# Kernel tuning notes

Measured on AMD Instinct MI355X. Metric: run time of the kernel, lower is better.

## Reference

```python
import jax, jax.numpy as jnp
import numpy as np

NUM_HEADS = 12
ROPE_THETA = 10000.0


def rope_angles(hd, end_x, end_y):
    # axial 2D rope angles, shape (L, hd//2); first hd//4 from x-coord, next hd//4 from y-coord
    f = 1.0 / (ROPE_THETA ** (np.arange(0, hd, 4)[: hd // 4].astype(np.float32) / hd))
    t = np.arange(end_x * end_y)
    tx = (t % end_x).astype(np.float32)
    ty = (t // end_x).astype(np.float32)
    ang = np.concatenate([np.outer(tx, f), np.outer(ty, f)], axis=-1)
    return jnp.asarray(ang, dtype=jnp.float32)


def apply_rope(q, ang):
    # q: (B, nH, L, hd); complex multiply on adjacent pairs
    cos, sin = jnp.cos(ang), jnp.sin(ang)  # (L, hd//2)
    qr = q.reshape(*q.shape[:-1], -1, 2)
    a, b = qr[..., 0], qr[..., 1]
    return jnp.stack([a * cos - b * sin, a * sin + b * cos], axis=-1).reshape(q.shape)


def setup_inputs() -> dict:
    key = jax.random.key(0)
    ks = jax.random.split(key, 7)
    dim, H, W, B = 768, 32, 32, 8
    hd = dim // NUM_HEADS
    return {
        "x": jax.random.normal(ks[0], (B, H, W, dim), jnp.float32),
        "qkv_w": jax.random.normal(ks[1], (3 * dim, dim), jnp.float32) * 0.02,
        "qkv_b": jax.random.normal(ks[2], (3 * dim,), jnp.float32) * 0.02,
        "proj_w": jax.random.normal(ks[3], (dim, dim), jnp.float32) * 0.02,
        "proj_b": jax.random.normal(ks[4], (dim,), jnp.float32) * 0.02,
        "rel_pos_h": jax.random.normal(ks[5], (2 * H - 1, hd), jnp.float32) * 0.02,
        "rel_pos_w": jax.random.normal(ks[6], (2 * W - 1, hd), jnp.float32) * 0.02,
    }


def reference(x, qkv_w, qkv_b, proj_w, proj_b, rel_pos_h, rel_pos_w):
    B, H, W, dim = x.shape
    nH = NUM_HEADS
    hd = dim // nH
    L = H * W
    qkv = jnp.einsum("blc,dc->bld", x.reshape(B, L, dim), qkv_w) + qkv_b
    qkv = qkv.reshape(B, L, 3, nH, hd)
    q = qkv[:, :, 0].transpose(0, 2, 1, 3)  # (B, nH, L, hd)
    k = qkv[:, :, 1].transpose(0, 2, 1, 3)
    v = qkv[:, :, 2].transpose(0, 2, 1, 3)
    # 2D rope (applied to both q and k)
    ang = rope_angles(hd, H, W)
    q = apply_rope(q, ang)
    k = apply_rope(k, ang)
    # relative position bias: equivalent math of concat_rel_pos(rescale=True) + SDPA
    # effective scores = (q.k)/sqrt(hd) + rel_h + rel_w
    rc = jnp.arange(H)[:, None] - jnp.arange(W)[None, :] + (H - 1)  # (H, W)
    Rh = rel_pos_h[rc]  # (H, K_h, hd)
    Rw = rel_pos_w[rc]  # (W, K_w, hd)
    rq = q.reshape(B, nH, H, W, hd)
    rel_h = jnp.einsum("bnhwc,hkc->bnhwk", rq, Rh)  # (B, nH, H, W, K_h)
    rel_w = jnp.einsum("bnhwc,wkc->bnhwk", rq, Rw)  # (B, nH, H, W, K_w)
    scores = jnp.einsum("bnqc,bnkc->bnqk", q, k) / jnp.sqrt(jnp.float32(hd))
    scores = scores.reshape(B, nH, H, W, H, W) + rel_h[..., :, None] + rel_w[..., None, :]
    attn = jax.nn.softmax(scores.reshape(B, nH, L, L), axis=-1)
    out = jnp.einsum("bnqk,bnkc->bnqc", attn, v)  # (B, nH, L, hd)
    out = out.transpose(0, 2, 1, 3).reshape(B, H, W, dim)
    return jnp.einsum("bhwc,dc->bhwd", out, proj_w) + proj_b
```

## Files before the change

### kernel.cpp

```cpp
#include <hip/hip_runtime.h>


typedef unsigned short u16;
typedef __attribute__((ext_vector_type(8))) __bf16 bf16x8;
typedef __attribute__((ext_vector_type(4))) float f32x4;
typedef __attribute__((address_space(1))) const unsigned int gu32;
typedef __attribute__((address_space(3))) unsigned int lu32;

#define LOG2E 1.4426950408889634f

__device__ __forceinline__ float b2f(u16 u) {
    unsigned int i = ((unsigned int)u) << 16;
    float f; __builtin_memcpy(&f, &i, 4); return f;
}
__device__ __forceinline__ u16 f2b(float f) {
    unsigned int x; __builtin_memcpy(&x, &f, 4);
    x += 0x7fffu + ((x >> 16) & 1u);
    return (u16)(x >> 16);
}

__global__ void detect_dtype(const u16* __restrict__ x, int* __restrict__ flag)
{
    if (threadIdx.x == 0 && blockIdx.x == 0) {
        float mx = 0.f;
        for (int i = 0; i < 128; i++) {
            float v = fabsf(b2f(x[i]));
            if (!(v <= 1e30f)) v = 1e30f;
            mx = fmaxf(mx, v);
        }
        *flag = (mx > 1e4f) ? 1 : 0;
    }
}

struct CvtArgs {
    const void* src[7];
    u16*        dst[7];
    int         n[7];
    float       sc[7];
};

__global__ __launch_bounds__(256) void convert_all(CvtArgs a, const int* __restrict__ flag)
{
    const int fl = *flag;
    const int g = blockIdx.x * 256 + threadIdx.x;
    const int stride = gridDim.x * 256;
    #pragma unroll 1
    for (int s = 0; s < 7; s++) {
        const int n = a.n[s];
        const float sc = a.sc[s];
        const float* fs = (const float*)a.src[s];
        const u16*  hs = (const u16*)a.src[s];
        u16* d = a.dst[s];
        for (int i = g; i < n; i += stride) {
            float v = fl ? fs[i] : b2f(hs[i]);
            d[i] = f2b(v * sc);
        }
    }
}

template <int EPI>
__global__ __launch_bounds__(256) void gemm128(
    const u16* __restrict__ A, const u16* __restrict__ Bw,
    const u16* __restrict__ bias, void* __restrict__ Cout,
    const int* __restrict__ flag, u16* __restrict__ qkvT, int N, int K)
{
    __shared__ __align__(16) u16 smem[16384];
    __shared__ float tabc[512];
    __shared__ float tabs[512];
    u16* lA = smem;
    u16* lB = smem + 8192;
    u16* ct = smem;
    const int tid = threadIdx.x;
    const int m0 = blockIdx.x * 128, n0 = blockIdx.y * 128;
    const int wave = tid >> 6, lane = tid & 63;
    const int wm = (wave & 1) * 64, wn = (wave >> 1) * 64;
    const int lm = lane & 15, lq = lane >> 4;
    const int srow = lane >> 3;
    const int sgcol = ((lane & 7) ^ (srow & 7)) * 8;
    const int sw0 = (lq ^ (lm & 7)) * 8;
    const int sw1 = ((lq + 4) ^ (lm & 7)) * 8;

    if (EPI == 1) {
        #pragma unroll
        for (int e = tid; e < 512; e += 256) {
            const int coord = e >> 4, jj = e & 15;
            const float ang = (float)coord * __expf(-(float)jj * 0.5756462732485115f);
            float sn, cs; __sincosf(ang, &sn, &cs);
            tabc[e] = cs; tabs[e] = sn;
        }
    }

    f32x4 acc[4][4] = {};
    for (int k0 = 0; k0 < K; k0 += 64) {
        if (k0) __syncthreads();
        #pragma unroll
        for (int c4 = 0; c4 < 4; c4++) {
            const int c = wave * 4 + c4;
            const int row = c * 8 + srow;
            __builtin_amdgcn_global_load_lds(
                (gu32*)(A + (size_t)(m0 + row) * K + k0 + sgcol),
                (lu32*)&lA[c * 512], 16, 0, 0);
            __builtin_amdgcn_global_load_lds(
                (gu32*)(Bw + (size_t)(n0 + row) * K + k0 + sgcol),
                (lu32*)&lB[c * 512], 16, 0, 0);
        }
        __syncthreads();
        #pragma unroll
        for (int ks = 0; ks < 64; ks += 32) {
            const int sw = ks ? sw1 : sw0;
            bf16x8 af[4], bfr[4];
            #pragma unroll
            for (int i = 0; i < 4; i++) af[i]  = *(const bf16x8*)&lA[(wm + i * 16 + lm) * 64 + sw];
            #pragma unroll
            for (int j = 0; j < 4; j++) bfr[j] = *(const bf16x8*)&lB[(wn + j * 16 + lm) * 64 + sw];
            #pragma unroll
            for (int i = 0; i < 4; i++)
                #pragma unroll
                for (int j = 0; j < 4; j++)
                    acc[i][j] = __builtin_amdgcn_mfma_f32_16x16x32_bf16(af[i], bfr[j], acc[i][j], 0, 0, 0);
        }
    }
    if (EPI == 0) {
        const int fl = *flag;
        #pragma unroll
        for (int j = 0; j < 4; j++) {
            const int n = n0 + wn + j * 16 + lm;
            const float bj = b2f(bias[n]);
            #pragma unroll
            for (int i = 0; i < 4; i++)
                #pragma unroll
                for (int r = 0; r < 4; r++) {
                    const int m = m0 + wm + i * 16 + lq * 4 + r;
                    const float v = acc[i][j][r] + bj;
                    if (fl) ((float*)Cout)[(size_t)m * 768 + n] = v;
                    else    ((u16*)Cout)[(size_t)m * 768 + n] = f2b(v);
                }
        }
    } else {
        const int which = n0 / 768;
        const bool vt = (which == 2);
        __syncthreads();
        #pragma unroll
        for (int j = 0; j < 4; j++) {
            const int nl = wn + j * 16 + lm;
            const int n = n0 + nl;
            const float bj = b2f(bias[n]);
            const int d = n & 63;
            const int pi = d >> 1;
            const int jj = pi & 15;
            #pragma unroll
            for (int i = 0; i < 4; i++)
                #pragma unroll
                for (int r = 0; r < 4; r++) {
                    const int ml = wm + i * 16 + lq * 4 + r;
                    const int m = m0 + ml;
                    float v = acc[i][j][r] + bj;
                    const float p = __shfl_xor(v, 1);
                    const int l = m & 1023;
                    float o = v;
                    if (which < 2) {
                        const int coord = (pi < 16) ? (l & 31) : (l >> 5);
                        const float cs = tabc[coord * 16 + jj];
                        const float sn = tabs[coord * 16 + jj];
                        o = v * cs + ((d & 1) ? p * sn : -(p * sn));
                        if (which == 1) o *= 0.125f * LOG2E;
                    }
                    ct[vt ? nl * 128 + ml : ml * 128 + nl] = f2b(o);
                }
        }
        __syncthreads();
        const size_t HL = (size_t)96 * 1024 * 64;
        const int nh0 = (n0 >> 6) % 12, bb = m0 >> 10, l0 = m0 & 1023;
        if (!vt) {
            #pragma unroll
            for (int pass = 0; pass < 8; pass++) {
                const int chunk = pass * 256 + tid;
                const int run = chunk >> 3, lc = chunk & 7;
                const int ml = run >> 1, h = run & 1;
                u16* gp = qkvT + (size_t)which * HL
                        + ((size_t)(bb * 12 + nh0 + h) * 1024 + l0 + ml) * 64 + lc * 8;
                *(uint4*)gp = *(const uint4*)&ct[ml * 128 + h * 64 + lc * 8];
            }
        } else {
            const int kt0 = l0 >> 6;
            #pragma unroll
            for (int pass = 0; pass < 8; pass++) {
                const int run = pass * 16 + (tid >> 4);
                const int ln = tid & 15;
                const int half = ln >> 3, l8 = ln & 7;
                u16* gp = qkvT + 2 * HL
                        + (size_t)(bb * 12 + nh0 + (run >> 6)) * 65536
                        + (size_t)(kt0 + half) * 4096 + (run & 63) * 64 + l8 * 8;
                *(uint4*)gp = *(const uint4*)&ct[run * 128 + ln * 8];
            }
        }
    }
}

__global__ __launch_bounds__(256, 3) void flash_attn_mfma(
    const u16* __restrict__ qkvT, const u16* __restrict__ relH,
    const u16* __restrict__ relW, u16* __restrict__ outb)
{
    __shared__ __align__(16) u16 ks2[2 * 4096];
    __shared__ __align__(16) u16 vsT[2 * 4096];
    __shared__ __align__(16) u16 ps[4096];
    __shared__ __align__(16) u16 ThL[128 * 36];
    u16* rel = vsT;
    u16* TwS = ks2;

    const int tid = threadIdx.x;
    const int w = tid >> 6, lane = tid & 63;
    const int lm = lane & 15, lq = lane >> 4;
    const int whi = (w >= 2) ? 1 : 0;
    const int srow = lane >> 3;
    const int sgcol = ((lane & 7) ^ (srow & 7)) * 8;
    const int sw0 = (lq ^ (lm & 7)) * 8;
    const int sw1 = ((lq + 4) ^ (lm & 7)) * 8;

    const int bn = blockIdx.x, q0 = blockIdx.y * 128;
    const int qh0 = blockIdx.y * 4;
    const size_t HL = (size_t)96 * 1024 * 64;
    const u16* qg  = qkvT + (size_t)bn * 65536 + (size_t)q0 * 64;
    const u16* kgb = qkvT + HL + (size_t)bn * 65536;
    const u16* vgb = qkvT + 2 * HL + (size_t)bn * 65536;

    bf16x8 bq0[2], bq1[2];
    #pragma unroll
    for (int h = 0; h < 2; h++) {
        const u16* qr = qg + (h * 64 + w * 16 + lm) * 64;
        bq0[h] = *(const bf16x8*)(qr + lq * 8);
        bq1[h] = *(const bf16x8*)(qr + 32 + lq * 8);
    }

    for (int g = tid; g < 1008; g += 256) {
        int r = g >> 4, c = (g & 15) * 4;
        *(ushort4*)&rel[r * 64 + c] = *(const ushort4*)(relH + g * 4);
    }
    if (tid < 16) { ushort4 z = {0, 0, 0, 0}; *(ushort4*)&rel[63 * 64 + tid * 4] = z; }
    __syncthreads();

    {
        #pragma unroll
        for (int h = 0; h < 2; h++) {
            f32x4 tacc[4] = {};
            #pragma unroll
            for (int nb = 0; nb < 4; nb++) {
                bf16x8 r0 = *(const bf16x8*)&rel[(nb * 16 + lm) * 64 + lq * 8];
                bf16x8 r1 = *(const bf16x8*)&rel[(nb * 16 + lm) * 64 + 32 + lq * 8];
                tacc[nb] = __builtin_amdgcn_mfma_f32_16x16x32_bf16(bq0[h], r0, tacc[nb], 0, 0, 0);
                tacc[nb] = __builtin_amdgcn_mfma_f32_16x16x32_bf16(bq1[h], r1, tacc[nb], 0, 0, 0);
            }
            #pragma unroll
            for (int nb = 0; nb < 4; nb++)
                #pragma unroll
                for (int rr = 0; rr < 4; rr++) {
                    const unsigned cw = (unsigned)(nb * 16 + lm - qh0);
                    if (cw < 36u)
                        ThL[(h * 64 + w * 16 + lq * 4 + rr) * 36 + cw] = f2b(tacc[nb][rr]);
                }
        }
    }
    __syncthreads();
    for (int g = tid; g < 1008; g += 256) {
        int r = g >> 4, c = (g & 15) * 4;
        *(ushort4*)&rel[r * 64 + c] = *(const ushort4*)(relW + g * 4);
    }
    if (tid < 16) { ushort4 z = {0, 0, 0, 0}; *(ushort4*)&rel[63 * 64 + tid * 4] = z; }
    __syncthreads();
    {
        #pragma unroll
        for (int h = 0; h < 2; h++) {
            f32x4 tacc[4] = {};
            #pragma unroll
            for (int nb = 0; nb < 4; nb++) {
                bf16x8 r0 = *(const bf16x8*)&rel[(nb * 16 + lm) * 64 + lq * 8];
                bf16x8 r1 = *(const bf16x8*)&rel[(nb * 16 + lm) * 64 + 32 + lq * 8];
                tacc[nb] = __builtin_amdgcn_mfma_f32_16x16x32_bf16(bq0[h], r0, tacc[nb], 0, 0, 0);
                tacc[nb] = __builtin_amdgcn_mfma_f32_16x16x32_bf16(bq1[h], r1, tacc[nb], 0, 0, 0);
            }
            #pragma unroll
            for (int nb = 0; nb < 4; nb++)
                #pragma unroll
                for (int rr = 0; rr < 4; rr++)
                    TwS[(h * 64 + w * 16 + lq * 4 + rr) * 64 + nb * 16 + lm] = f2b(tacc[nb][rr]);
        }
    }
    __syncthreads();
    const int qw = (w & 1) * 16 + lm;
    float rwc[2][8];
    #pragma unroll
    for (int h = 0; h < 2; h++)
        #pragma unroll
        for (int mb2 = 0; mb2 < 2; mb2++)
            #pragma unroll
            for (int rr = 0; rr < 4; rr++) {
                const int kw = mb2 * 16 + lq * 4 + rr;
                rwc[h][mb2 * 4 + rr] =
                    b2f(TwS[(h * 64 + w * 16 + lm) * 64 + qw - kw + 31]) - 16.0f;
            }

    union { unsigned u[4]; bf16x8 v; } uo;
    uo.u[0] = uo.u[1] = uo.u[2] = uo.u[3] = 0x3F803F80u;
    const bf16x8 vone = uo.v;

    f32x4 lacc[2] = {};
    f32x4 oacc[2][4] = {};

    __syncthreads();
    #pragma unroll
    for (int c4 = 0; c4 < 2; c4++) {
        const int c = w * 2 + c4;
        const int row = c * 8 + srow;
        __builtin_amdgcn_global_load_lds(
            (gu32*)(kgb + row * 64 + sgcol), (lu32*)&ks2[c * 512], 16, 0, 0);
        __builtin_amdgcn_global_load_lds(
            (gu32*)(vgb + row * 64 + sgcol), (lu32*)&vsT[c * 512], 16, 0, 0);
    }

    #pragma unroll 1
    for (int kt = 0; kt < 16; kt++) {
        __syncthreads();
        const int bo = (kt & 1) * 4096;
        if (kt < 15) {
            const int bn1 = ((kt + 1) & 1) * 4096;
            const u16* kp = kgb + (size_t)(kt + 1) * 4096;
            const u16* vp = vgb + (size_t)(kt + 1) * 4096;
            #pragma unroll
            for (int c4 = 0; c4 < 2; c4++) {
                const int c = w * 2 + c4;
                const int row = c * 8 + srow;
                __builtin_amdgcn_global_load_lds(
                    (gu32*)(kp + row * 64 + sgcol), (lu32*)&ks2[bn1 + c * 512], 16, 0, 0);
                __builtin_amdgcn_global_load_lds(
                    (gu32*)(vp + row * 64 + sgcol), (lu32*)&vsT[bn1 + c * 512], 16, 0, 0);
            }
        }
        float rh[2][2];
        #pragma unroll
        for (int h = 0; h < 2; h++) {
            const int colp = h * 2 + whi - 2 * kt + 31;
            rh[h][0] = b2f(ThL[(h * 64 + w * 16 + lm) * 36 + colp]);
            rh[h][1] = b2f(ThL[(h * 64 + w * 16 + lm) * 36 + colp - 1]);
        }
        bf16x8 ka0[4], ka1[4];
        #pragma unroll
        for (int mb = 0; mb < 4; mb++) {
            ka0[mb] = *(const bf16x8*)&ks2[bo + (mb * 16 + lm) * 64 + sw0];
            ka1[mb] = *(const bf16x8*)&ks2[bo + (mb * 16 + lm) * 64 + sw1];
        }
        #pragma unroll
        for (int h = 0; h < 2; h++) {
            f32x4 sacc[4];
            #pragma unroll
            for (int mb = 0; mb < 4; mb++) {
                #pragma unroll
                for (int j = 0; j < 4; j++)
                    sacc[mb][j] = rh[h][mb >> 1] + rwc[h][(mb & 1) * 4 + j];
                sacc[mb] = __builtin_amdgcn_mfma_f32_16x16x32_bf16(ka0[mb], bq0[h], sacc[mb], 0, 0, 0);
                sacc[mb] = __builtin_amdgcn_mfma_f32_16x16x32_bf16(ka1[mb], bq1[h], sacc[mb], 0, 0, 0);
            }
            #pragma unroll
            for (int mb = 0; mb < 4; mb++) {
                float p0 = exp2f(sacc[mb][0]);
                float p1 = exp2f(sacc[mb][1]);
                float p2 = exp2f(sacc[mb][2]);
                float p3 = exp2f(sacc[mb][3]);
                unsigned w0, w1;
                asm("v_cvt_pk_bf16_f32 %0, %1, %2" : "=v"(w0) : "v"(p0), "v"(p1));
                asm("v_cvt_pk_bf16_f32 %0, %1, %2" : "=v"(w1) : "v"(p2), "v"(p3));
                uint2 u; u.x = w0; u.y = w1;
                const int gg = 2 * mb + (lq >> 1);
                *(uint2*)&ps[(w * 16 + lm) * 64 + ((gg ^ (lm & 7)) * 8) + (lq & 1) * 4] = u;
            }
            const bf16x8 pa0 = *(const bf16x8*)&ps[(w * 16 + lm) * 64 + sw0];
            const bf16x8 pa1 = *(const bf16x8*)&ps[(w * 16 + lm) * 64 + sw1];
            lacc[h] = __builtin_amdgcn_mfma_f32_16x16x32_bf16(pa0, vone, lacc[h], 0, 0, 0);
            lacc[h] = __builtin_amdgcn_mfma_f32_16x16x32_bf16(pa1, vone, lacc[h], 0, 0, 0);
            #pragma unroll
            for (int nb = 0; nb < 4; nb++) {
                bf16x8 vb0 = *(const bf16x8*)&vsT[bo + (nb * 16 + lm) * 64 + sw0];
                bf16x8 vb1 = *(const bf16x8*)&vsT[bo + (nb * 16 + lm) * 64 + sw1];
                oacc[h][nb] = __builtin_amdgcn_mfma_f32_16x16x32_bf16(pa0, vb0, oacc[h][nb], 0, 0, 0);
                oacc[h][nb] = __builtin_amdgcn_mfma_f32_16x16x32_bf16(pa1, vb1, oacc[h][nb], 0, 0, 0);
            }
        }
    }
    const int bb = bn / 12, nh = bn % 12;
    #pragma unroll
    for (int h = 0; h < 2; h++) {
        float rv[4];
        #pragma unroll
        for (int rr = 0; rr < 4; rr++) rv[rr] = 1.f / lacc[h][rr];
        #pragma unroll
        for (int nb = 0; nb < 4; nb++)
            #pragma unroll
            for (int rr = 0; rr < 4; rr++) {
                const int qrow = q0 + h * 64 + w * 16 + lq * 4 + rr;
                const int d = nb * 16 + lm;
                outb[((size_t)(bb * 1024 + qrow)) * 768 + nh * 64 + d] =
                    f2b(oacc[h][nb][rr] * rv[rr]);
            }
    }
}

extern "C" void kernel_launch(void* const* d_in, const int* in_sizes, int n_in,
                              void* d_out, int out_size, void* d_ws, size_t ws_size,
                              hipStream_t stream)
{
    u16* ws16  = (u16*)d_ws;
    u16* qkvT  = ws16;
    u16* xb    = ws16 + (size_t)18874368;
    u16* attn  = xb;
    const size_t S = 25165824;
    u16* qkvw_b = ws16 + S;
    u16* projw_b = qkvw_b + 1769472;
    u16* qkvb_b = projw_b + 589824;
    u16* projb_b = qkvb_b + 2304;
    u16* relh_b = projb_b + 768;
    u16* relw_b = relh_b + 4032;
    int* flag = (int*)(ws16 + S + 2370432);

    detect_dtype<<<1, 64, 0, stream>>>((const u16*)d_in[0], flag);

    CvtArgs ca;
    ca.src[0] = d_in[0]; ca.dst[0] = xb;      ca.n[0] = 6291456; ca.sc[0] = 1.0f;
    ca.src[1] = d_in[1]; ca.dst[1] = qkvw_b;  ca.n[1] = 1769472; ca.sc[1] = 1.0f;
    ca.src[2] = d_in[3]; ca.dst[2] = projw_b; ca.n[2] = 589824;  ca.sc[2] = 1.0f;
    ca.src[3] = d_in[2]; ca.dst[3] = qkvb_b;  ca.n[3] = 2304;    ca.sc[3] = 1.0f;
    ca.src[4] = d_in[4]; ca.dst[4] = projb_b; ca.n[4] = 768;     ca.sc[4] = 1.0f;
    ca.src[5] = d_in[5]; ca.dst[5] = relh_b;  ca.n[5] = 4032;    ca.sc[5] = LOG2E;
    ca.src[6] = d_in[6]; ca.dst[6] = relw_b;  ca.n[6] = 4032;    ca.sc[6] = LOG2E;
    convert_all<<<2048, 256, 0, stream>>>(ca, flag);

    gemm128<1><<<dim3(64, 18), 256, 0, stream>>>(xb, qkvw_b, qkvb_b, nullptr, flag, qkvT, 2304, 768);
    flash_attn_mfma<<<dim3(96, 8), 256, 0, stream>>>(qkvT, relh_b, relw_b, attn);
    gemm128<0><<<dim3(64, 6), 256, 0, stream>>>(attn, projw_b, projb_b, d_out, flag, nullptr, 768, 768);
}
```

Before: 225.1 us.

## Double-buffer GEMM K-tiles in LDS with prefetch of next tile

The 128x128 GEMM main loop now uses K-tiles of 32 instead of 64 and splits the same shared buffer into two halves. The next tile is issued with global_load_lds while MFMAs run on the current one. This is meant to hide global-load latency behind compute and to drop one of the two barriers per iteration. In exchange there are twice as many loop iterations, a new swizzle pattern for the narrower rows, and a single barrier per step whose correctness depends on the load-to-LDS ordering.

```diff
diff --git a/kernel.cpp b/kernel.cpp
--- a/kernel.cpp
+++ b/kernel.cpp
@@ -67,18 +67,15 @@
     __shared__ __align__(16) u16 smem[16384];
     __shared__ float tabc[512];
     __shared__ float tabs[512];
-    u16* lA = smem;
-    u16* lB = smem + 8192;
     u16* ct = smem;
     const int tid = threadIdx.x;
     const int m0 = blockIdx.x * 128, n0 = blockIdx.y * 128;
     const int wave = tid >> 6, lane = tid & 63;
     const int wm = (wave & 1) * 64, wn = (wave >> 1) * 64;
     const int lm = lane & 15, lq = lane >> 4;
-    const int srow = lane >> 3;
-    const int sgcol = ((lane & 7) ^ (srow & 7)) * 8;
-    const int sw0 = (lq ^ (lm & 7)) * 8;
-    const int sw1 = ((lq + 4) ^ (lm & 7)) * 8;
+    const int qr  = lane >> 2;
+    const int scg = ((lane & 3) ^ (qr & 3)) * 8;
+    const int rsw = (lq ^ (lm & 3)) * 8;
 
     if (EPI == 1) {
         #pragma unroll
@@ -90,36 +87,51 @@
         }
     }
 
+    const int nkt = K >> 5;
+    #pragma unroll
+    for (int c4 = 0; c4 < 2; c4++) {
+        const int c = wave * 2 + c4;
+        const int row = c * 16 + qr;
+        __builtin_amdgcn_global_load_lds(
+            (gu32*)(A + (size_t)(m0 + row) * K + scg),
+            (lu32*)&smem[c * 512], 16, 0, 0);
+        __builtin_amdgcn_global_load_lds(
+            (gu32*)(Bw + (size_t)(n0 + row) * K + scg),
+            (lu32*)&smem[4096 + c * 512], 16, 0, 0);
+    }
+
     f32x4 acc[4][4] = {};
-    for (int k0 = 0; k0 < K; k0 += 64) {
-        if (k0) __syncthreads();
-        #pragma unroll
-        for (int c4 = 0; c4 < 4; c4++) {
-            const int c = wave * 4 + c4;
-            const int row = c * 8 + srow;
-            __builtin_amdgcn_global_load_lds(
-                (gu32*)(A + (size_t)(m0 + row) * K + k0 + sgcol),
-                (lu32*)&lA[c * 512], 16, 0, 0);
-            __builtin_amdgcn_global_load_lds(
-                (gu32*)(Bw + (size_t)(n0 + row) * K + k0 + sgcol),
-                (lu32*)&lB[c * 512], 16, 0, 0);
-        }
+    #pragma unroll 1
+    for (int kt = 0; kt < nkt; kt++) {
         __syncthreads();
-        #pragma unroll
-        for (int ks = 0; ks < 64; ks += 32) {
-            const int sw = ks ? sw1 : sw0;
-            bf16x8 af[4], bfr[4];
-            #pragma unroll
-            for (int i = 0; i < 4; i++) af[i]  = *(const bf16x8*)&lA[(wm + i * 16 + lm) * 64 + sw];
-            #pragma unroll
-            for (int j = 0; j < 4; j++) bfr[j] = *(const bf16x8*)&lB[(wn + j * 16 + lm) * 64 + sw];
-            #pragma unroll
-            for (int i = 0; i < 4; i++)
-                #pragma unroll
-                for (int j = 0; j < 4; j++)
-                    acc[i][j] = __builtin_amdgcn_mfma_f32_16x16x32_bf16(af[i], bfr[j], acc[i][j], 0, 0, 0);
-        }
-    }
+        const int bo = (kt & 1) * 8192;
+        if (kt + 1 < nkt) {
+            const int bn1 = ((kt + 1) & 1) * 8192;
+            const int k1 = (kt + 1) * 32;
+            #pragma unroll
+            for (int c4 = 0; c4 < 2; c4++) {
+                const int c = wave * 2 + c4;
+                const int row = c * 16 + qr;
+                __builtin_amdgcn_global_load_lds(
+                    (gu32*)(A + (size_t)(m0 + row) * K + k1 + scg),
+                    (lu32*)&smem[bn1 + c * 512], 16, 0, 0);
+                __builtin_amdgcn_global_load_lds(
+                    (gu32*)(Bw + (size_t)(n0 + row) * K + k1 + scg),
+                    (lu32*)&smem[bn1 + 4096 + c * 512], 16, 0, 0);
+            }
+        }
+        bf16x8 af[4], bfr[4];
+        #pragma unroll
+        for (int i = 0; i < 4; i++) af[i]  = *(const bf16x8*)&smem[bo + (wm + i * 16 + lm) * 32 + rsw];
+        #pragma unroll
+        for (int j = 0; j < 4; j++) bfr[j] = *(const bf16x8*)&smem[bo + 4096 + (wn + j * 16 + lm) * 32 + rsw];
+        #pragma unroll
+        for (int i = 0; i < 4; i++)
+            #pragma unroll
+            for (int j = 0; j < 4; j++)
+                acc[i][j] = __builtin_amdgcn_mfma_f32_16x16x32_bf16(af[i], bfr[j], acc[i][j], 0, 0, 0);
+    }
+
     if (EPI == 0) {
         const int fl = *flag;
         #pragma unroll
@@ -227,9 +239,9 @@
     bf16x8 bq0[2], bq1[2];
     #pragma unroll
     for (int h = 0; h < 2; h++) {
-        const u16* qr = qg + (h * 64 + w * 16 + lm) * 64;
-        bq0[h] = *(const bf16x8*)(qr + lq * 8);
-        bq1[h] = *(const bf16x8*)(qr + 32 + lq * 8);
+        const u16* qr2 = qg + (h * 64 + w * 16 + lm) * 64;
+        bq0[h] = *(const bf16x8*)(qr2 + lq * 8);
+        bq1[h] = *(const bf16x8*)(qr2 + 32 + lq * 8);
     }
 
     for (int g = tid; g < 1008; g += 256) {
```

After: 218.1 us. -3.1%, faster.
